# Kernel tuning notes

Hardware: AMD Instinct MI355X
Metric: run time of the kernel (lower is better)

Reference implementation:

```python
import math
import jax, jax.numpy as jnp
import numpy as np

B, T, C, H = 2, 2048, 1024, 16
HD = C // H  # head dim = 64


def setup_inputs() -> dict:
    key = jax.random.key(0)
    k1, k2, k3 = jax.random.split(key, 3)
    x = jax.random.normal(k1, (B, T, C), dtype=jnp.float32)
    w_attn = jax.random.normal(k2, (C, 3 * C), dtype=jnp.float32) * (1.0 / math.sqrt(C))
    b_attn = jnp.zeros((3 * C,), dtype=jnp.float32)
    w_proj = jax.random.normal(k3, (C, C), dtype=jnp.float32) * (1.0 / math.sqrt(C))
    b_proj = jnp.zeros((C,), dtype=jnp.float32)
    return {"x": x, "w_attn": w_attn, "b_attn": b_attn, "w_proj": w_proj, "b_proj": b_proj}


def reference(x, w_attn, b_attn, w_proj, b_proj):
    b, t, c = x.shape
    hd = c // H
    # fused QKV projection: [B,T,3C]
    qkv = x @ w_attn + b_attn
    q, k, v = jnp.split(qkv, 3, axis=2)
    # [B,T,C] -> [B,H,T,hd]
    q = q.reshape(b, t, H, hd).transpose(0, 2, 1, 3)
    k = k.reshape(b, t, H, hd).transpose(0, 2, 1, 3)
    v = v.reshape(b, t, H, hd).transpose(0, 2, 1, 3)
    # scaled scores: [B,H,T,T]
    att = jnp.einsum("bhqd,bhkd->bhqk", q, k) * (1.0 / math.sqrt(hd))
    # causal mask: keep lower triangle, -inf elsewhere
    causal = jnp.tril(jnp.ones((t, t), dtype=bool))
    att = jnp.where(causal[None, None, :, :], att, jnp.float32(-jnp.inf))
    att = jax.nn.softmax(att, axis=-1)
    # attention-weighted values: [B,H,T,hd] -> [B,T,C]
    y = jnp.einsum("bhqk,bhkd->bhqd", att, v)
    y = y.transpose(0, 2, 1, 3).reshape(b, t, c)
    # output projection (dropout prob 0 => identity)
    return y @ w_proj + b_proj
```

## Files before the change

### kernel.cpp

```cpp
#include <hip/hip_runtime.h>


typedef __bf16 bf16x8 __attribute__((ext_vector_type(8)));
typedef __bf16 bf16x4 __attribute__((ext_vector_type(4)));
typedef short shortx4 __attribute__((ext_vector_type(4)));
typedef float f32x4 __attribute__((ext_vector_type(4)));

#define B_ 2
#define T_ 2048
#define C_ 1024
#define H_ 16
#define HD_ 64
#define ROWS_ (B_ * T_)
#define N3C_ (3 * C_)

__device__ inline void gll16(const void* g, void* l) {
    __builtin_amdgcn_global_load_lds(
        (const __attribute__((address_space(1))) void*)g,
        (__attribute__((address_space(3))) void*)l, 16, 0, 0);
}

__device__ inline f32x4 mfma16x16x16(bf16x4 a, bf16x4 b, f32x4 c) {
#if defined(__HIP_DEVICE_COMPILE__)
#if __has_builtin(__builtin_amdgcn_mfma_f32_16x16x16bf16_1k)
    return __builtin_amdgcn_mfma_f32_16x16x16bf16_1k(
        __builtin_bit_cast(shortx4, a), __builtin_bit_cast(shortx4, b), c, 0, 0, 0);
#else
    return __builtin_amdgcn_mfma_f32_16x16x16_bf16(
        __builtin_bit_cast(shortx4, a), __builtin_bit_cast(shortx4, b), c, 0, 0, 0);
#endif
#else
    (void)a; (void)b;
    return c;
#endif
}

__global__ void detect_dtype(const unsigned* __restrict__ w, unsigned* __restrict__ flag) {
    int lane = threadIdx.x & 63;
    int cnt = 0;
#pragma unroll
    for (int i = 0; i < 4; ++i) {
        unsigned v = w[lane * 4 + i];
        unsigned e = (v >> 7) & 0xFFu;
        cnt += (e >= 116u && e <= 134u) ? 1 : 0;
    }
#pragma unroll
    for (int off = 1; off < 64; off <<= 1) cnt += __shfl_xor(cnt, off, 64);
    if (lane == 0) *flag = (cnt >= 128) ? 1u : 0u;
}

__global__ __launch_bounds__(256) void convert_to_bf16(const void* __restrict__ src,
                                                       __bf16* __restrict__ dst, int n,
                                                       const unsigned* __restrict__ flag) {
    bool isbf = (*flag != 0u);
    int i = (blockIdx.x * 256 + threadIdx.x) * 8;
    if (i >= n) return;
    if (isbf) {
        *(bf16x8*)&dst[i] = *(const bf16x8*)((const __bf16*)src + i);
    } else {
        const float4* s4 = (const float4*)src;
        float4 a = s4[i / 4], b = s4[i / 4 + 1];
        bf16x8 v;
        v[0] = (__bf16)a.x; v[1] = (__bf16)a.y; v[2] = (__bf16)a.z; v[3] = (__bf16)a.w;
        v[4] = (__bf16)b.x; v[5] = (__bf16)b.y; v[6] = (__bf16)b.z; v[7] = (__bf16)b.w;
        *(bf16x8*)&dst[i] = v;
    }
}

__global__ __launch_bounds__(256) void transpose_conv(const void* __restrict__ src,
                                                      __bf16* __restrict__ dst,
                                                      int R, int Cc,
                                                      const unsigned* __restrict__ flag) {
    __shared__ __align__(16) __bf16 tile[64][65];
    bool isbf = (*flag != 0u);
    const __bf16* sb = (const __bf16*)src;
    const float* sf = (const float*)src;
    int cb = blockIdx.x * 64, rb = blockIdx.y * 64;
    for (int i = threadIdx.x; i < 4096; i += 256) {
        int r = i >> 6, c = i & 63;
        size_t idx = (size_t)(rb + r) * Cc + cb + c;
        tile[r][c] = isbf ? sb[idx] : (__bf16)sf[idx];
    }
    __syncthreads();
    for (int i = threadIdx.x; i < 4096; i += 256) {
        int r = i >> 6, c = i & 63;
        dst[(size_t)(cb + r) * R + rb + c] = tile[c][r];
    }
}

__global__ __launch_bounds__(256) void gemm_qkv(const __bf16* __restrict__ A,
                                                const __bf16* __restrict__ Bt,
                                                const __bf16* __restrict__ bias,
                                                __bf16* __restrict__ qg,
                                                __bf16* __restrict__ kg,
                                                __bf16* __restrict__ vtg) {
    const int K = C_;
    __shared__ __align__(16) __bf16 As[128 * 32];
    __shared__ __align__(16) __bf16 Bs[128 * 32];
    int tid = threadIdx.x;
    int wave = tid >> 6, lane = tid & 63;
    int quad = lane >> 4, l15 = lane & 15;
    int mb = blockIdx.y * 128, nb = blockIdx.x * 128;
    int wm = (wave >> 1) * 64, wn = (wave & 1) * 64;

    f32x4 acc[4][4] = {};

    for (int k0 = 0; k0 < K; k0 += 32) {
        __syncthreads();
#pragma unroll
        for (int q = 0; q < 2; ++q) {
            int id = q * 256 + tid;
            int r = id >> 2, c8 = (id & 3) * 8;
            gll16(&A[(size_t)(mb + r) * K + k0 + c8], &As[(q * 256 + wave * 64) * 8]);
            gll16(&Bt[(size_t)(nb + r) * K + k0 + c8], &Bs[(q * 256 + wave * 64) * 8]);
        }
        __syncthreads();

        bf16x8 af[4], bfr[4];
#pragma unroll
        for (int i = 0; i < 4; ++i)
            af[i] = *(const bf16x8*)&As[(wm + i * 16 + l15) * 32 + quad * 8];
#pragma unroll
        for (int j = 0; j < 4; ++j)
            bfr[j] = *(const bf16x8*)&Bs[(wn + j * 16 + l15) * 32 + quad * 8];
#pragma unroll
        for (int i = 0; i < 4; ++i)
#pragma unroll
            for (int j = 0; j < 4; ++j)
                acc[i][j] = __builtin_amdgcn_mfma_f32_16x16x32_bf16(af[i], bfr[j], acc[i][j], 0, 0, 0);
    }

#pragma unroll
    for (int i = 0; i < 4; ++i) {
        int row = mb + wm + i * 16 + quad * 4;
#pragma unroll
        for (int j = 0; j < 4; ++j) {
            int col = nb + wn + j * 16 + l15;
            float bv = (float)bias[col];
            int region = col >> 10;
            int cc = col & 1023;
            int hh = cc >> 6, hd = cc & 63;
#pragma unroll
            for (int r = 0; r < 4; ++r) {
                int rr = row + r;
                int t = rr & (T_ - 1), bb = rr >> 11;
                float val = acc[i][j][r] + bv;
                size_t bh = (size_t)(bb * H_ + hh);
                if (region == 0)      qg[(bh * T_ + t) * HD_ + hd] = (__bf16)val;
                else if (region == 1) kg[(bh * T_ + t) * HD_ + hd] = (__bf16)val;
                else                  vtg[(bh * HD_ + hd) * T_ + t] = (__bf16)val;
            }
        }
    }
}

__global__ __launch_bounds__(128) void attn_kernel(const __bf16* __restrict__ qg,
                                                   const __bf16* __restrict__ kg,
                                                   const __bf16* __restrict__ vtg,
                                                   __bf16* __restrict__ y) {
    const int LDT = 72;
    __shared__ __align__(16) __bf16 Ks[64 * LDT];
    __shared__ __align__(16) __bf16 Vts[64 * LDT];

    int tid = threadIdx.x, wave = tid >> 6, lane = tid & 63;
    int quad = lane >> 4, l15 = lane & 15;
    int px = blockIdx.x;
    int p = px >> 1, half = px & 1;
    int qA = p, qB = 31 - p;
    int bh = blockIdx.y;
    int b = bh >> 4, h = bh & 15;

    const __bf16* qbh = qg + (size_t)bh * T_ * HD_;
    const __bf16* kbh = kg + (size_t)bh * T_ * HD_;
    const __bf16* vbh = vtg + (size_t)bh * HD_ * T_;

    int rowA = qA * 64 + half * 32 + wave * 16;
    int rowB = qB * 64 + half * 32 + wave * 16;

    bf16x8 qfA[2], qfB[2];
#pragma unroll
    for (int ks = 0; ks < 2; ++ks) {
        qfA[ks] = *(const bf16x8*)&qbh[(size_t)(rowA + l15) * HD_ + ks * 32 + quad * 8];
        qfB[ks] = *(const bf16x8*)&qbh[(size_t)(rowB + l15) * HD_ + ks * 32 + quad * 8];
    }

    f32x4 oA[4] = {}, oB[4] = {};
    float lA = 0.f, lB = 0.f;
    const float M = 12.0f;

    bf16x8 kf[4][2];
    bf16x4 vf[4][4];

    auto tile_step = [&](const bf16x8* qf, int rowX, int kbase, bool diag,
                         f32x4* o, float& l) {
        f32x4 s[4] = {};
#pragma unroll
        for (int ks = 0; ks < 2; ++ks)
#pragma unroll
            for (int j = 0; j < 4; ++j)
                s[j] = __builtin_amdgcn_mfma_f32_16x16x32_bf16(kf[j][ks], qf[ks], s[j], 0, 0, 0);

        int q = rowX + l15;
#pragma unroll
        for (int j = 0; j < 4; ++j) {
            bf16x4 pb;
#pragma unroll
            for (int r = 0; r < 4; ++r) {
                int key = kbase + j * 16 + quad * 4 + r;
                float x = s[j][r] * 0.125f - M;
                float e = (diag && key > q) ? 0.f : __expf(x);
                pb[r] = (__bf16)e;
                l += (float)pb[r];
            }
#pragma unroll
            for (int i = 0; i < 4; ++i)
                o[i] = mfma16x16x16(pb, vf[i][j], o[i]);
        }
    };

    for (int kt = 0; kt <= qB; ++kt) {
        int kbase = kt * 64;
        __syncthreads();
#pragma unroll
        for (int t = 0; t < 4; ++t) {
            int vid = tid + t * 128;
            int r = vid >> 3, c = (vid & 7) * 8;
            *(bf16x8*)&Ks[r * LDT + c]  = *(const bf16x8*)&kbh[(size_t)(kbase + r) * HD_ + c];
            *(bf16x8*)&Vts[r * LDT + c] = *(const bf16x8*)&vbh[(size_t)r * T_ + kbase + c];
        }
        __syncthreads();

#pragma unroll
        for (int j = 0; j < 4; ++j)
#pragma unroll
            for (int ks = 0; ks < 2; ++ks)
                kf[j][ks] = *(const bf16x8*)&Ks[(j * 16 + l15) * LDT + ks * 32 + quad * 8];
#pragma unroll
        for (int i = 0; i < 4; ++i)
#pragma unroll
            for (int j = 0; j < 4; ++j)
                vf[i][j] = *(const bf16x4*)&Vts[(i * 16 + l15) * LDT + j * 16 + quad * 4];

        tile_step(qfB, rowB, kbase, kt == qB, oB, lB);
        if (kt <= qA)
            tile_step(qfA, rowA, kbase, kt == qA, oA, lA);
    }

    lA += __shfl_xor(lA, 16, 64); lA += __shfl_xor(lA, 32, 64);
    lB += __shfl_xor(lB, 16, 64); lB += __shfl_xor(lB, 32, 64);
    float rlA[4], rlB[4];
#pragma unroll
    for (int r = 0; r < 4; ++r) {
        rlA[r] = __shfl(lA, quad * 4 + r, 16);
        rlB[r] = __shfl(lB, quad * 4 + r, 16);
    }

#pragma unroll
    for (int i = 0; i < 4; ++i) {
        int col = h * HD_ + i * 16 + l15;
#pragma unroll
        for (int r = 0; r < 4; ++r) {
            y[(size_t)(b * T_ + rowA + quad * 4 + r) * C_ + col] = (__bf16)(oA[i][r] / rlA[r]);
            y[(size_t)(b * T_ + rowB + quad * 4 + r) * C_ + col] = (__bf16)(oB[i][r] / rlB[r]);
        }
    }
}

__global__ __launch_bounds__(256) void gemm_bt_bias(const __bf16* __restrict__ A,
                                                    const __bf16* __restrict__ Bt,
                                                    const __bf16* __restrict__ bias,
                                                    void* __restrict__ Cv,
                                                    int M, int N, int K,
                                                    const unsigned* __restrict__ flag) {
    __shared__ __align__(16) __bf16 As[128 * 32];
    __shared__ __align__(16) __bf16 Bs[128 * 32];
    bool out_bf = (*flag != 0u);
    int tid = threadIdx.x;
    int wave = tid >> 6, lane = tid & 63;
    int quad = lane >> 4, l15 = lane & 15;
    int mb = blockIdx.y * 128, nb = blockIdx.x * 128;
    int wm = (wave >> 1) * 64, wn = (wave & 1) * 64;

    f32x4 acc[4][4] = {};

    for (int k0 = 0; k0 < K; k0 += 32) {
        __syncthreads();
#pragma unroll
        for (int q = 0; q < 2; ++q) {
            int id = q * 256 + tid;
            int r = id >> 2, c8 = (id & 3) * 8;
            gll16(&A[(size_t)(mb + r) * K + k0 + c8], &As[(q * 256 + wave * 64) * 8]);
            gll16(&Bt[(size_t)(nb + r) * K + k0 + c8], &Bs[(q * 256 + wave * 64) * 8]);
        }
        __syncthreads();

        bf16x8 af[4], bfr[4];
#pragma unroll
        for (int i = 0; i < 4; ++i)
            af[i] = *(const bf16x8*)&As[(wm + i * 16 + l15) * 32 + quad * 8];
#pragma unroll
        for (int j = 0; j < 4; ++j)
            bfr[j] = *(const bf16x8*)&Bs[(wn + j * 16 + l15) * 32 + quad * 8];
#pragma unroll
        for (int i = 0; i < 4; ++i)
#pragma unroll
            for (int j = 0; j < 4; ++j)
                acc[i][j] = __builtin_amdgcn_mfma_f32_16x16x32_bf16(af[i], bfr[j], acc[i][j], 0, 0, 0);
    }

#pragma unroll
    for (int i = 0; i < 4; ++i) {
        int row = mb + wm + i * 16 + quad * 4;
#pragma unroll
        for (int j = 0; j < 4; ++j) {
            int col = nb + wn + j * 16 + l15;
            float bv = (float)bias[col];
#pragma unroll
            for (int r = 0; r < 4; ++r) {
                float val = acc[i][j][r] + bv;
                size_t off = (size_t)(row + r) * N + col;
                if (out_bf) ((__bf16*)Cv)[off] = (__bf16)val;
                else        ((float*)Cv)[off]  = val;
            }
        }
    }
}

extern "C" void kernel_launch(void* const* d_in, const int* in_sizes, int n_in,
                              void* d_out, int out_size, void* d_ws, size_t ws_size,
                              hipStream_t stream) {
    const void* x      = d_in[0];
    const void* w_attn = d_in[1];
    const void* b_attn = d_in[2];
    const void* w_proj = d_in[3];
    const void* b_proj = d_in[4];

    char* base = (char*)d_ws;
    unsigned* flag = (unsigned*)base;
    __bf16* xc   = (__bf16*)(base + 256);
    __bf16* wat  = xc + (size_t)ROWS_ * C_;
    __bf16* wpt  = wat + (size_t)N3C_ * C_;
    __bf16* bac  = wpt + (size_t)C_ * C_;
    __bf16* bpc  = bac + N3C_;
    __bf16* qg   = bpc + C_;
    __bf16* kg   = qg + (size_t)B_ * H_ * T_ * HD_;
    __bf16* vtg  = kg + (size_t)B_ * H_ * T_ * HD_;
    __bf16* yb   = vtg + (size_t)B_ * H_ * T_ * HD_;

    detect_dtype<<<1, 64, 0, stream>>>((const unsigned*)x, flag);

    convert_to_bf16<<<(ROWS_ * C_ / 8 + 255) / 256, 256, 0, stream>>>(x, xc, ROWS_ * C_, flag);
    convert_to_bf16<<<(N3C_ / 8 + 255) / 256, 256, 0, stream>>>(b_attn, bac, N3C_, flag);
    convert_to_bf16<<<(C_ / 8 + 255) / 256, 256, 0, stream>>>(b_proj, bpc, C_, flag);

    transpose_conv<<<dim3(N3C_ / 64, C_ / 64), 256, 0, stream>>>(w_attn, wat, C_, N3C_, flag);
    transpose_conv<<<dim3(C_ / 64, C_ / 64), 256, 0, stream>>>(w_proj, wpt, C_, C_, flag);

    gemm_qkv<<<dim3(N3C_ / 128, ROWS_ / 128), 256, 0, stream>>>(xc, wat, bac, qg, kg, vtg);

    attn_kernel<<<dim3(32, B_ * H_), 128, 0, stream>>>(qg, kg, vtg, yb);

    gemm_bt_bias<<<dim3(C_ / 128, ROWS_ / 128), 256, 0, stream>>>(
        yb, wpt, bpc, d_out, ROWS_, C_, C_, flag);
}
```

Before: 221.5 us.

## Merge prep kernels, move softmax row-sum to MFMA, shrink proj GEMM tile

```diff
diff --git a/kernel.cpp b/kernel.cpp
--- a/kernel.cpp
+++ b/kernel.cpp
@@ -1,4 +1,5 @@
 #include <hip/hip_runtime.h>
+#include <type_traits>
 
 
 typedef __bf16 bf16x8 __attribute__((ext_vector_type(8)));
@@ -33,6 +34,10 @@
     (void)a; (void)b;
     return c;
 #endif
+}
+
+__device__ inline float bias_at(const void* bias, int col, bool in_bf) {
+    return in_bf ? (float)((const __bf16*)bias)[col] : ((const float*)bias)[col];
 }
 
 __global__ void detect_dtype(const unsigned* __restrict__ w, unsigned* __restrict__ flag) {
@@ -67,10 +72,17 @@
     }
 }
 
-__global__ __launch_bounds__(256) void transpose_conv(const void* __restrict__ src,
-                                                      __bf16* __restrict__ dst,
-                                                      int R, int Cc,
-                                                      const unsigned* __restrict__ flag) {
+__global__ __launch_bounds__(256) void transpose2(const void* __restrict__ wa,
+                                                  __bf16* __restrict__ wat,
+                                                  const void* __restrict__ wp,
+                                                  __bf16* __restrict__ wpt,
+                                                  const unsigned* __restrict__ flag) {
+    int z = blockIdx.z;
+    if (z && blockIdx.x >= 16) return;
+    const void* src = z ? wp : wa;
+    __bf16* dst = z ? wpt : wat;
+    int R = C_, Cc = z ? C_ : N3C_;
+
     __shared__ __align__(16) __bf16 tile[64][65];
     bool isbf = (*flag != 0u);
     const __bf16* sb = (const __bf16*)src;
@@ -90,13 +102,15 @@
 
 __global__ __launch_bounds__(256) void gemm_qkv(const __bf16* __restrict__ A,
                                                 const __bf16* __restrict__ Bt,
-                                                const __bf16* __restrict__ bias,
+                                                const void* __restrict__ bias,
                                                 __bf16* __restrict__ qg,
                                                 __bf16* __restrict__ kg,
-                                                __bf16* __restrict__ vtg) {
+                                                __bf16* __restrict__ vtg,
+                                                const unsigned* __restrict__ flag) {
     const int K = C_;
     __shared__ __align__(16) __bf16 As[128 * 32];
     __shared__ __align__(16) __bf16 Bs[128 * 32];
+    bool in_bf = (*flag != 0u);
     int tid = threadIdx.x;
     int wave = tid >> 6, lane = tid & 63;
     int quad = lane >> 4, l15 = lane & 15;
@@ -136,7 +150,7 @@
 #pragma unroll
         for (int j = 0; j < 4; ++j) {
             int col = nb + wn + j * 16 + l15;
-            float bv = (float)bias[col];
+            float bv = bias_at(bias, col, in_bf);
             int region = col >> 10;
             int cc = col & 1023;
             int hh = cc >> 6, hd = cc & 63;
@@ -185,14 +199,20 @@
     }
 
     f32x4 oA[4] = {}, oB[4] = {};
-    float lA = 0.f, lB = 0.f;
-    const float M = 12.0f;
+    f32x4 laccA = {}, laccB = {};
+    const float C1 = 0.125f * 1.44269504088896340736f;
+    const float C2 = 12.0f * 1.44269504088896340736f;
+
+    bf16x4 onesb;
+#pragma unroll
+    for (int e = 0; e < 4; ++e) onesb[e] = (__bf16)1.0f;
 
     bf16x8 kf[4][2];
     bf16x4 vf[4][4];
 
-    auto tile_step = [&](const bf16x8* qf, int rowX, int kbase, bool diag,
-                         f32x4* o, float& l) {
+    auto tile_step = [&](auto diagc, const bf16x8* qf, int rowX, int kbase,
+                         f32x4* o, f32x4& lacc) {
+        constexpr bool DIAG = decltype(diagc)::value;
         f32x4 s[4] = {};
 #pragma unroll
         for (int ks = 0; ks < 2; ++ks)
@@ -206,15 +226,17 @@
             bf16x4 pb;
 #pragma unroll
             for (int r = 0; r < 4; ++r) {
-                int key = kbase + j * 16 + quad * 4 + r;
-                float x = s[j][r] * 0.125f - M;
-                float e = (diag && key > q) ? 0.f : __expf(x);
+                float e = exp2f(fmaf(s[j][r], C1, -C2));
+                if (DIAG) {
+                    int key = kbase + j * 16 + quad * 4 + r;
+                    e = (key > q) ? 0.f : e;
+                }
                 pb[r] = (__bf16)e;
-                l += (float)pb[r];
             }
 #pragma unroll
             for (int i = 0; i < 4; ++i)
                 o[i] = mfma16x16x16(pb, vf[i][j], o[i]);
+            lacc = mfma16x16x16(pb, onesb, lacc);
         }
     };
 
@@ -241,18 +263,10 @@
             for (int j = 0; j < 4; ++j)
                 vf[i][j] = *(const bf16x4*)&Vts[(i * 16 + l15) * LDT + j * 16 + quad * 4];
 
-        tile_step(qfB, rowB, kbase, kt == qB, oB, lB);
-        if (kt <= qA)
-            tile_step(qfA, rowA, kbase, kt == qA, oA, lA);
-    }
-
-    lA += __shfl_xor(lA, 16, 64); lA += __shfl_xor(lA, 32, 64);
-    lB += __shfl_xor(lB, 16, 64); lB += __shfl_xor(lB, 32, 64);
-    float rlA[4], rlB[4];
-#pragma unroll
-    for (int r = 0; r < 4; ++r) {
-        rlA[r] = __shfl(lA, quad * 4 + r, 16);
-        rlB[r] = __shfl(lB, quad * 4 + r, 16);
+        if (kt == qB) tile_step(std::true_type{},  qfB, rowB, kbase, oB, laccB);
+        else          tile_step(std::false_type{}, qfB, rowB, kbase, oB, laccB);
+        if (kt < qA)       tile_step(std::false_type{}, qfA, rowA, kbase, oA, laccA);
+        else if (kt == qA) tile_step(std::true_type{},  qfA, rowA, kbase, oA, laccA);
     }
 
 #pragma unroll
@@ -260,67 +274,70 @@
         int col = h * HD_ + i * 16 + l15;
 #pragma unroll
         for (int r = 0; r < 4; ++r) {
-            y[(size_t)(b * T_ + rowA + quad * 4 + r) * C_ + col] = (__bf16)(oA[i][r] / rlA[r]);
-            y[(size_t)(b * T_ + rowB + quad * 4 + r) * C_ + col] = (__bf16)(oB[i][r] / rlB[r]);
-        }
-    }
-}
-
-__global__ __launch_bounds__(256) void gemm_bt_bias(const __bf16* __restrict__ A,
-                                                    const __bf16* __restrict__ Bt,
-                                                    const __bf16* __restrict__ bias,
-                                                    void* __restrict__ Cv,
-                                                    int M, int N, int K,
-                                                    const unsigned* __restrict__ flag) {
-    __shared__ __align__(16) __bf16 As[128 * 32];
+            y[(size_t)(b * T_ + rowA + quad * 4 + r) * C_ + col] = (__bf16)(oA[i][r] / laccA[r]);
+            y[(size_t)(b * T_ + rowB + quad * 4 + r) * C_ + col] = (__bf16)(oB[i][r] / laccB[r]);
+        }
+    }
+}
+
+__global__ __launch_bounds__(256) void gemm_proj(const __bf16* __restrict__ A,
+                                                 const __bf16* __restrict__ Bt,
+                                                 const void* __restrict__ bias,
+                                                 void* __restrict__ Cv,
+                                                 const unsigned* __restrict__ flag) {
+    const int K = C_, N = C_;
+    __shared__ __align__(16) __bf16 As[64 * 32];
     __shared__ __align__(16) __bf16 Bs[128 * 32];
-    bool out_bf = (*flag != 0u);
+    bool in_bf = (*flag != 0u);
     int tid = threadIdx.x;
     int wave = tid >> 6, lane = tid & 63;
     int quad = lane >> 4, l15 = lane & 15;
-    int mb = blockIdx.y * 128, nb = blockIdx.x * 128;
-    int wm = (wave >> 1) * 64, wn = (wave & 1) * 64;
-
-    f32x4 acc[4][4] = {};
+    int mb = blockIdx.y * 64, nb = blockIdx.x * 128;
+    int wm = (wave >> 1) * 32, wn = (wave & 1) * 64;
+
+    f32x4 acc[2][4] = {};
 
     for (int k0 = 0; k0 < K; k0 += 32) {
         __syncthreads();
+        {
+            int r = tid >> 2, c8 = (tid & 3) * 8;
+            gll16(&A[(size_t)(mb + r) * K + k0 + c8], &As[(wave * 64) * 8]);
+        }
 #pragma unroll
         for (int q = 0; q < 2; ++q) {
             int id = q * 256 + tid;
             int r = id >> 2, c8 = (id & 3) * 8;
-            gll16(&A[(size_t)(mb + r) * K + k0 + c8], &As[(q * 256 + wave * 64) * 8]);
             gll16(&Bt[(size_t)(nb + r) * K + k0 + c8], &Bs[(q * 256 + wave * 64) * 8]);
         }
         __syncthreads();
 
-        bf16x8 af[4], bfr[4];
-#pragma unroll
-        for (int i = 0; i < 4; ++i)
+        bf16x8 af[2], bfr[4];
+#pragma unroll
+        for (int i = 0; i < 2; ++i)
             af[i] = *(const bf16x8*)&As[(wm + i * 16 + l15) * 32 + quad * 8];
 #pragma unroll
         for (int j = 0; j < 4; ++j)
             bfr[j] = *(const bf16x8*)&Bs[(wn + j * 16 + l15) * 32 + quad * 8];
 #pragma unroll
-        for (int i = 0; i < 4; ++i)
+        for (int i = 0; i < 2; ++i)
 #pragma unroll
             for (int j = 0; j < 4; ++j)
                 acc[i][j] = __builtin_amdgcn_mfma_f32_16x16x32_bf16(af[i], bfr[j], acc[i][j], 0, 0, 0);
     }
 
 #pragma unroll
-    for (int i = 0; i < 4; ++i) {
+    for (int i = 0; i < 2; ++i) {
         int row = mb + wm + i * 16 + quad * 4;
 #pragma unroll
         for (int j = 0; j < 4; ++j) {
             int col = nb + wn + j * 16 + l15;
-            float bv = (float)bias[col];
+            float bv = bias_at(bias, col, in_bf);
 #pragma unroll
             for (int r = 0; r < 4; ++r) {
                 float val = acc[i][j][r] + bv;
                 size_t off = (size_t)(row + r) * N + col;
-                if (out_bf) ((__bf16*)Cv)[off] = (__bf16)val;
-                else        ((float*)Cv)[off]  = val;
+                if (in_bf) ((__bf16*)Cv)[off] = (__bf16)val;
+                else       ((float*)Cv)[off]  = val;
             }
         }
     }
@@ -340,9 +357,7 @@
     __bf16* xc   = (__bf16*)(base + 256);
     __bf16* wat  = xc + (size_t)ROWS_ * C_;
     __bf16* wpt  = wat + (size_t)N3C_ * C_;
-    __bf16* bac  = wpt + (size_t)C_ * C_;
-    __bf16* bpc  = bac + N3C_;
-    __bf16* qg   = bpc + C_;
+    __bf16* qg   = wpt + (size_t)C_ * C_;
     __bf16* kg   = qg + (size_t)B_ * H_ * T_ * HD_;
     __bf16* vtg  = kg + (size_t)B_ * H_ * T_ * HD_;
     __bf16* yb   = vtg + (size_t)B_ * H_ * T_ * HD_;
@@ -350,16 +365,13 @@
     detect_dtype<<<1, 64, 0, stream>>>((const unsigned*)x, flag);
 
     convert_to_bf16<<<(ROWS_ * C_ / 8 + 255) / 256, 256, 0, stream>>>(x, xc, ROWS_ * C_, flag);
-    convert_to_bf16<<<(N3C_ / 8 + 255) / 256, 256, 0, stream>>>(b_attn, bac, N3C_, flag);
-    convert_to_bf16<<<(C_ / 8 + 255) / 256, 256, 0, stream>>>(b_proj, bpc, C_, flag);
-
-    transpose_conv<<<dim3(N3C_ / 64, C_ / 64), 256, 0, stream>>>(w_attn, wat, C_, N3C_, flag);
-    transpose_conv<<<dim3(C_ / 64, C_ / 64), 256, 0, stream>>>(w_proj, wpt, C_, C_, flag);
-
-    gemm_qkv<<<dim3(N3C_ / 128, ROWS_ / 128), 256, 0, stream>>>(xc, wat, bac, qg, kg, vtg);
+
+    transpose2<<<dim3(N3C_ / 64, C_ / 64, 2), 256, 0, stream>>>(w_attn, wat, w_proj, wpt, flag);
+
+    gemm_qkv<<<dim3(N3C_ / 128, ROWS_ / 128), 256, 0, stream>>>(
+        xc, wat, b_attn, qg, kg, vtg, flag);
 
     attn_kernel<<<dim3(32, B_ * H_), 128, 0, stream>>>(qg, kg, vtg, yb);
 
-    gemm_bt_bias<<<dim3(C_ / 128, ROWS_ / 128), 256, 0, stream>>>(
-        yb, wpt, bpc, d_out, ROWS_, C_, C_, flag);
-}
+    gemm_proj<<<dim3(C_ / 128, ROWS_ / 64), 256, 0, stream>>>(yb, wpt, b_proj, d_out, flag);
+}
```

Measured after the change: 209.3 us. 1.06x faster.
